# Kernel tuning notes

Measured on AMD Instinct MI355X. Metric: run time of the kernel, lower is better.

The kernel has to match this reference:

```python
import jax, jax.numpy as jnp
from jax import lax
import numpy as np

B, COND_C = 16, 256
IN_C, OUT_C, K = 64, 64, 3
H = W = 128
N_PARAM = K * K * IN_C * OUT_C + OUT_C  # 36928


def setup_inputs() -> dict:
    key = jax.random.key(0)
    k1, k2, k3, k4 = jax.random.split(key, 4)
    x = jax.random.normal(k1, (B, IN_C, H, W), dtype=jnp.float32)
    conditioning = jax.random.normal(k2, (B, COND_C), dtype=jnp.float32)
    # nn.Linear(cond_c, n_param): weight [n_param, cond_c], bias [n_param]
    W_cond = jax.random.normal(k3, (N_PARAM, COND_C), dtype=jnp.float32) * 0.02
    b_cond = jax.random.normal(k4, (N_PARAM,), dtype=jnp.float32) * 0.02
    return {"x": x, "conditioning": conditioning, "W_cond": W_cond, "b_cond": b_cond}


def reference(x, conditioning, W_cond, b_cond):
    # Hypernetwork: Linear + tanh*5 (ConditionerActivation)
    w_b = jnp.tanh(conditioning @ W_cond.T + b_cond) * 5.0  # [B, N_PARAM]
    bias = w_b[:, -OUT_C:]                                   # [B, out_c]
    w = w_b[:, :-OUT_C].reshape(B, OUT_C, IN_C, K, K)        # per-sample OIHW

    def conv_one(xi, wi, bi):
        # xi: [in_c, H, W], wi: [out_c, in_c, K, K], bi: [out_c]
        y = lax.conv_general_dilated(
            xi[None], wi,
            window_strides=(1, 1),
            padding=[(1, 1), (1, 1)],
            dimension_numbers=("NCHW", "OIHW", "NCHW"),
        )[0]
        return y + bi[:, None, None]

    return jax.vmap(conv_one)(x, w, bias)  # [B, out_c, H, W]
```

## Files before the change

kernel.cpp:

```cpp
#include <hip/hip_runtime.h>
#include <math.h>
#include <stdint.h>

#define B_    16
#define CONDC 256
#define ICn   64
#define OCn   64
#define Hn    128
#define Wn    128
#define NW    36864
#define NPARAM 36928

typedef _Float16 half8 __attribute__((ext_vector_type(8)));
typedef _Float16 half4 __attribute__((ext_vector_type(4)));
typedef float f32x4 __attribute__((ext_vector_type(4)));
typedef float f32x16 __attribute__((ext_vector_type(16)));

__device__ inline unsigned pk2(float a, float b) {
    union { _Float16 h[2]; unsigned u; } q;
    q.h[0] = (_Float16)a; q.h[1] = (_Float16)b;
    return q.u;
}

__global__ void transpose_k(const float* __restrict__ x, _Float16* __restrict__ xt) {
    __shared__ unsigned ls[4160];
    const int tid = threadIdx.x;
    const int bx  = blockIdx.x;

    if (bx < 2048) {
        const int b = bx >> 7, y = bx & 127;
        const float* xrow = x + (size_t)b * 1048576 + (size_t)y * 128;

        float4 va[4], vb[4];
        #pragma unroll
        for (int t = 0; t < 4; ++t) {
            int u = t * 256 + tid;
            int icp = u >> 5, xg = u & 31;
            const float* r0 = xrow + (size_t)(2 * icp) * 16384;
            va[t] = *((const float4*)r0 + xg);
            vb[t] = *((const float4*)(r0 + 16384) + xg);
        }
        __builtin_amdgcn_sched_barrier(0);

        #pragma unroll
        for (int t = 0; t < 4; ++t) {
            int u = t * 256 + tid;
            int icp = u >> 5, xg = u & 31;
            unsigned* dst = ls + icp * 130 + 4 * xg;
            *(uint2*)(dst)     = make_uint2(pk2(va[t].x, vb[t].x), pk2(va[t].y, vb[t].y));
            *(uint2*)(dst + 2) = make_uint2(pk2(va[t].z, vb[t].z), pk2(va[t].w, vb[t].w));
        }
        __syncthreads();

        _Float16* rowhalf = xt + (size_t)(b * 130 + y + 1) * 8320;
        #pragma unroll
        for (int t = 0; t < 5; ++t) {
            int u = t * 256 + tid;
            if (u < 1040) {
                int xp = u >> 3, g = u & 7;
                uint4 val = make_uint4(0u, 0u, 0u, 0u);
                if (xp > 0 && xp < 129) {
                    int xx = xp - 1;
                    val.x = ls[(4 * g + 0) * 130 + xx];
                    val.y = ls[(4 * g + 1) * 130 + xx];
                    val.z = ls[(4 * g + 2) * 130 + xx];
                    val.w = ls[(4 * g + 3) * 130 + xx];
                }
                *(uint4*)(rowhalf + (size_t)u * 8) = val;
            }
        }
    } else {
        const int q = bx - 2048;
        const int b = q >> 1, yp = (q & 1) ? 129 : 0;
        _Float16* rowhalf = xt + (size_t)(b * 130 + yp) * 8320;
        uint4 z = make_uint4(0u, 0u, 0u, 0u);
        for (int u = tid; u < 1040; u += 256)
            *(uint4*)(rowhalf + (size_t)u * 8) = z;
    }
}

__global__ __launch_bounds__(256, 4) void gemm_k(const float* __restrict__ cond,
                                                 const float* __restrict__ Wc,
                                                 const float* __restrict__ bc,
                                                 _Float16* __restrict__ wt,
                                                 float* __restrict__ bias) {
    __shared__ _Float16 wl[64 * 280];
    const int tid = threadIdx.x;
    const int pbase = blockIdx.x * 64;

    float4 v[16];
    #pragma unroll
    for (int t = 0; t < 16; ++t) {
        int u = t * 256 + tid;
        int pl = u >> 6, kg = u & 63;
        v[t] = *((const float4*)(Wc + (size_t)(pbase + pl) * 256) + kg);
    }
    __builtin_amdgcn_sched_barrier(0);

    #pragma unroll
    for (int t = 0; t < 16; ++t) {
        int u = t * 256 + tid;
        int pl = u >> 6, kg = u & 63;
        half4 h = { (_Float16)v[t].x, (_Float16)v[t].y, (_Float16)v[t].z, (_Float16)v[t].w };
        *(half4*)(wl + pl * 280 + kg * 4) = h;
    }
    __syncthreads();

    const int w = tid >> 6, l = tid & 63, n = l & 15, r4 = l >> 4;
    const _Float16* arow = wl + (w * 16 + n) * 280 + r4 * 8;
    const float*    crow = cond + n * 256 + r4 * 8;
    f32x4 acc = (f32x4){0.f, 0.f, 0.f, 0.f};
    #pragma unroll
    for (int kk = 0; kk < 8; ++kk) {
        half8 av = *(const half8*)(arow + kk * 32);
        float4 u0 = *(const float4*)(crow + kk * 32);
        float4 u1 = *(const float4*)(crow + kk * 32 + 4);
        half8 bv;
        bv[0] = (_Float16)u0.x; bv[1] = (_Float16)u0.y; bv[2] = (_Float16)u0.z; bv[3] = (_Float16)u0.w;
        bv[4] = (_Float16)u1.x; bv[5] = (_Float16)u1.y; bv[6] = (_Float16)u1.z; bv[7] = (_Float16)u1.w;
        acc = __builtin_amdgcn_mfma_f32_16x16x32_f16(av, bv, acc, 0, 0, 0);
    }
    #pragma unroll
    for (int j = 0; j < 4; ++j) {
        int p = pbase + w * 16 + r4 * 4 + j;
        float vv = tanhf(acc[j] + bc[p]) * 5.0f;
        if (p < NW) {
            int oc = p / 576, rem = p - oc * 576;
            int ic = rem / 9,  t  = rem - ic * 9;
            int icq = ic >> 4, icl = ic & 15;
            wt[((((size_t)n * 4 + icq) * 9 + t) * 64 + oc) * 16 + icl] = (_Float16)vv;
        } else {
            bias[n * 64 + (p - NW)] = vv;
        }
    }
}

__global__ __launch_bounds__(512, 2) void conv_v4(const _Float16* __restrict__ xt,
                                                  const _Float16* __restrict__ wt,
                                                  const float* __restrict__ bias,
                                                  float* __restrict__ out) {
    __shared__ _Float16 xs[2][12288];
    const int tid = threadIdx.x;
    const int l   = tid & 63;
    const int w   = tid >> 6;
    const int px  = l & 31;
    const int jj  = l >> 5;
    const int ot  = w & 1;
    const int rg  = w >> 1;
    const int b   = blockIdx.z;
    const int X0  = blockIdx.x * 32;
    const int Y0g = blockIdx.y * 16;

    const _Float16* xbase = xt + ((size_t)(b * 130 + Y0g) * 130 + X0) * 64;
    const _Float16* wbat  = wt + (size_t)b * 36864 + (size_t)(ot * 32 + px) * 16 + jj * 8;

    int offkw[3];
    #pragma unroll
    for (int kw = 0; kw < 3; ++kw) {
        int c = (px + kw) * 2 + jj;
        offkw[kw] = (c ^ ((c >> 3) & 7)) * 16;
    }
    const int Lb = rg * 4;

    #define STAGEQ(ICQ, BUF) do {                                                       \
        _Pragma("unroll")                                                               \
        for (int it = 0; it < 3; ++it) {                                                \
            int d  = it * 512 + tid;                                                    \
            int dc = d < 1296 ? d : 1295;                                               \
            int row = (int)((unsigned)dc / 72u);                                        \
            int c   = dc - row * 72;                                                    \
            int cs  = c ^ ((c >> 3) & 7);                                               \
            const _Float16* src = xbase + (size_t)row * 8320 + (cs >> 1) * 64           \
                                + (ICQ) * 16 + (cs & 1) * 8;                            \
            __builtin_amdgcn_global_load_lds(                                           \
                (const __attribute__((address_space(1))) void*)src,                     \
                (__attribute__((address_space(3))) void*)((__attribute__((address_space(3))) char*)xs + (BUF) * 24576 + (it * 512 + (tid & ~63)) * 16), \
                16, 0, 0);                                                              \
        } } while (0)

    STAGEQ(0, 0);
    half8 A[2][9];
    #pragma unroll
    for (int t = 0; t < 9; ++t) A[0][t] = *(const half8*)(wbat + t * 1024);

    f32x16 acc[4];
    #pragma unroll
    for (int r = 0; r < 4; ++r) acc[r] = (f32x16){};

    #pragma unroll
    for (int icq = 0; icq < 4; ++icq) {
        const int cur = icq & 1;
        if (icq < 3) {
            STAGEQ(icq + 1, cur ^ 1);
            asm volatile("s_waitcnt vmcnt(3)" ::: "memory");
        } else {
            asm volatile("s_waitcnt vmcnt(0)" ::: "memory");
        }
        __builtin_amdgcn_sched_barrier(0);
        __builtin_amdgcn_s_barrier();
        __builtin_amdgcn_sched_barrier(0);

        if (icq < 3) {
            #pragma unroll
            for (int t = 0; t < 9; ++t)
                A[cur ^ 1][t] = *(const half8*)(wbat + ((icq + 1) * 9 + t) * 1024);
        }

        const char* bufb = (const char*)xs + cur * 24576;
        #pragma unroll
        for (int kw = 0; kw < 3; ++kw) {
            half8 Bf[6];
            #pragma unroll
            for (int iy = 0; iy < 6; ++iy)
                Bf[iy] = *(const half8*)(bufb + (Lb + iy) * 1152 + offkw[kw]);
            #pragma unroll
            for (int iy = 0; iy < 6; ++iy) {
                #pragma unroll
                for (int kh = 0; kh < 3; ++kh) {
                    const int r = iy - kh;
                    if (r >= 0 && r < 4)
                        acc[r] = __builtin_amdgcn_mfma_f32_32x32x16_f16(A[cur][kh * 3 + kw], Bf[iy], acc[r], 0, 0, 0);
                }
            }
        }
        asm volatile("s_waitcnt lgkmcnt(0)" ::: "memory");
        __builtin_amdgcn_sched_barrier(0);
        __builtin_amdgcn_s_barrier();
        __builtin_amdgcn_sched_barrier(0);
    }
    #undef STAGEQ

    const float* bb = bias + b * 64;
    #pragma unroll
    for (int r = 0; r < 4; ++r) {
        const int yo = Y0g + Lb + r;
        float* ob = out + (((size_t)(b * 64 + ot * 32)) * 128 + yo) * 128 + X0 + px;
        #pragma unroll
        for (int reg = 0; reg < 16; ++reg) {
            const int ocl = (reg & 3) + 8 * (reg >> 2) + 4 * jj;
            ob[(size_t)ocl * 16384] = acc[r][reg] + bb[ot * 32 + ocl];
        }
    }
}

__global__ __launch_bounds__(256) void cond_gemm(const float* __restrict__ cond,
                                                 const float* __restrict__ Wc,
                                                 const float* __restrict__ bc,
                                                 float* __restrict__ wb) {
    __shared__ float condl[B_][CONDC + 1];
    __shared__ float Wl[16][CONDC + 1];
    const int tid = threadIdx.x;
    const int p0 = blockIdx.x * 16;
    for (int i = tid; i < B_ * CONDC; i += 256) condl[i >> 8][i & 255] = cond[i];
    for (int i = tid; i < 16 * CONDC; i += 256) {
        int pl = i >> 8, k = i & 255;
        Wl[pl][k] = Wc[(p0 + pl) * CONDC + k];
    }
    __syncthreads();
    const int pl = tid >> 4;
    const int b  = tid & 15;
    float acc = bc[p0 + pl];
    #pragma unroll 8
    for (int k = 0; k < CONDC; ++k) acc += Wl[pl][k] * condl[b][k];
    wb[b * NPARAM + p0 + pl] = tanhf(acc) * 5.0f;
}

#define TS  32
#define OG  8
#define ICC 8
__global__ __launch_bounds__(256) void conv_kernel(const float* __restrict__ x,
                                                   const float* __restrict__ wb,
                                                   float* __restrict__ out) {
    __shared__ float fxs[ICC][TS + 2][TS + 2];
    __shared__ float ws[OG][ICC][9];
    const int tid = threadIdx.x;
    const int b   = blockIdx.z;
    const int ocg = blockIdx.y * OG;
    const int tx0 = (blockIdx.x & 3) * TS;
    const int ty0 = (blockIdx.x >> 2) * TS;
    const int px  = (tid & 15) * 2;
    const int py  = (tid >> 4) * 2;
    float acc[OG][4];
    #pragma unroll
    for (int o = 0; o < OG; ++o)
        #pragma unroll
        for (int q = 0; q < 4; ++q) acc[o][q] = 0.0f;
    const float* wbase = wb + b * NPARAM;
    for (int ic0 = 0; ic0 < ICn; ic0 += ICC) {
        for (int i = tid; i < ICC * (TS + 2) * (TS + 2); i += 256) {
            int icl = i / ((TS + 2) * (TS + 2));
            int rem = i % ((TS + 2) * (TS + 2));
            int yy = rem / (TS + 2), xx = rem % (TS + 2);
            int gy = ty0 - 1 + yy, gx = tx0 - 1 + xx;
            float v = 0.0f;
            if (gy >= 0 && gy < Hn && gx >= 0 && gx < Wn)
                v = x[((b * ICn + ic0 + icl) * Hn + gy) * Wn + gx];
            fxs[icl][yy][xx] = v;
        }
        for (int i = tid; i < OG * ICC * 9; i += 256) {
            int o = i / (ICC * 9), rem = i % (ICC * 9);
            int icl = rem / 9, k = rem % 9;
            ws[o][icl][k] = wbase[((ocg + o) * ICn + ic0 + icl) * 9 + k];
        }
        __syncthreads();
        #pragma unroll
        for (int icl = 0; icl < ICC; ++icl) {
            float xv[4][4];
            #pragma unroll
            for (int dy = 0; dy < 4; ++dy)
                #pragma unroll
                for (int dx = 0; dx < 4; ++dx) xv[dy][dx] = fxs[icl][py + dy][px + dx];
            #pragma unroll
            for (int o = 0; o < OG; ++o)
                #pragma unroll
                for (int kh = 0; kh < 3; ++kh)
                    #pragma unroll
                    for (int kw = 0; kw < 3; ++kw) {
                        float wv = ws[o][icl][kh * 3 + kw];
                        acc[o][0] += xv[kh][kw] * wv;
                        acc[o][1] += xv[kh][kw + 1] * wv;
                        acc[o][2] += xv[kh + 1][kw] * wv;
                        acc[o][3] += xv[kh + 1][kw + 1] * wv;
                    }
        }
        __syncthreads();
    }
    #pragma unroll
    for (int o = 0; o < OG; ++o) {
        float bias = wbase[NW + ocg + o];
        int oc = ocg + o;
        float* obase = out + ((size_t)(b * OCn + oc) * Hn + (ty0 + py)) * Wn + tx0 + px;
        obase[0] = acc[o][0] + bias;
        obase[1] = acc[o][1] + bias;
        obase[Wn] = acc[o][2] + bias;
        obase[Wn + 1] = acc[o][3] + bias;
    }
}

extern "C" void kernel_launch(void* const* d_in, const int* in_sizes, int n_in,
                              void* d_out, int out_size, void* d_ws, size_t ws_size,
                              hipStream_t stream) {
    const float* x    = (const float*)d_in[0];
    const float* cond = (const float*)d_in[1];
    const float* Wc   = (const float*)d_in[2];
    const float* bc   = (const float*)d_in[3];
    float* out = (float*)d_out;

    const size_t WT_BYTES = (size_t)B_ * 9 * 64 * 64 * 2;
    const size_t BIAS_OFF = WT_BYTES;
    const size_t XT_OFF   = 1183744;
    const size_t XT_BYTES = (size_t)B_ * 130 * 130 * 64 * 2 + 32768;
    const size_t NEED     = XT_OFF + XT_BYTES;

    if (ws_size >= NEED) {
        _Float16* wt   = (_Float16*)d_ws;
        float*    bias = (float*)((char*)d_ws + BIAS_OFF);
        _Float16* xt   = (_Float16*)((char*)d_ws + XT_OFF);
        transpose_k<<<dim3(2048 + 32), 256, 0, stream>>>(x, xt);
        gemm_k<<<dim3(577), 256, 0, stream>>>(cond, Wc, bc, wt, bias);
        conv_v4<<<dim3(4, 8, 16), 512, 0, stream>>>(xt, wt, bias, out);
    } else {
        float* wbuf = (float*)d_ws;
        cond_gemm<<<dim3(NPARAM / 16), 256, 0, stream>>>(cond, Wc, bc, wbuf);
        conv_kernel<<<dim3(16, OCn / OG, B_), 256, 0, stream>>>(x, wbuf, out);
    }
}
```

Measured before the change: 69.94 us.

## Shrink conv tiles, triple-buffer input stages, and swizzle block order

The conv kernel now uses 256-thread blocks covering 8 output rows instead of 16, with a three-deep LDS ring of input channel-quarter stages in place of double buffering. All three first stages are prefetched up front, and the four channel quarters are explicitly unrolled with tuned vmcnt waits. A 1D grid with a swizzled block-to-tile mapping spreads consecutive blocks across batches. The goal is better latency hiding and more resident blocks, at the cost of more halo reloads from the smaller tiles and fragile hand-counted waitcnt values.

```diff
diff --git a/kernel.cpp b/kernel.cpp
--- a/kernel.cpp
+++ b/kernel.cpp
@@ -135,11 +135,11 @@
     }
 }
 
-__global__ __launch_bounds__(512, 2) void conv_v4(const _Float16* __restrict__ xt,
+__global__ __launch_bounds__(256, 3) void conv_v5(const _Float16* __restrict__ xt,
                                                   const _Float16* __restrict__ wt,
                                                   const float* __restrict__ bias,
                                                   float* __restrict__ out) {
-    __shared__ _Float16 xs[2][12288];
+    __shared__ _Float16 xs[3 * 6144];
     const int tid = threadIdx.x;
     const int l   = tid & 63;
     const int w   = tid >> 6;
@@ -147,9 +147,11 @@
     const int jj  = l >> 5;
     const int ot  = w & 1;
     const int rg  = w >> 1;
-    const int b   = blockIdx.z;
-    const int X0  = blockIdx.x * 32;
-    const int Y0g = blockIdx.y * 16;
+
+    const int sw = (blockIdx.x & 7) * 128 + (blockIdx.x >> 3);
+    const int Xt = sw & 3, Yt = (sw >> 2) & 15, b = sw >> 6;
+    const int X0  = Xt * 32;
+    const int Y0g = Yt * 8;
 
     const _Float16* xbase = xt + ((size_t)(b * 130 + Y0g) * 130 + X0) * 64;
     const _Float16* wbat  = wt + (size_t)b * 36864 + (size_t)(ot * 32 + px) * 16 + jj * 8;
@@ -165,70 +167,90 @@
     #define STAGEQ(ICQ, BUF) do {                                                       \
         _Pragma("unroll")                                                               \
         for (int it = 0; it < 3; ++it) {                                                \
-            int d  = it * 512 + tid;                                                    \
-            int dc = d < 1296 ? d : 1295;                                               \
-            int row = (int)((unsigned)dc / 72u);                                        \
-            int c   = dc - row * 72;                                                    \
+            int d   = it * 256 + tid;                                                   \
+            int row = (int)((unsigned)d / 72u);                                         \
+            int c   = d - row * 72;                                                     \
             int cs  = c ^ ((c >> 3) & 7);                                               \
             const _Float16* src = xbase + (size_t)row * 8320 + (cs >> 1) * 64           \
                                 + (ICQ) * 16 + (cs & 1) * 8;                            \
             __builtin_amdgcn_global_load_lds(                                           \
                 (const __attribute__((address_space(1))) void*)src,                     \
-                (__attribute__((address_space(3))) void*)((__attribute__((address_space(3))) char*)xs + (BUF) * 24576 + (it * 512 + (tid & ~63)) * 16), \
+                (__attribute__((address_space(3))) void*)((__attribute__((address_space(3))) char*)xs + (BUF) * 12288 + (it * 256 + (tid & ~63)) * 16), \
                 16, 0, 0);                                                              \
         } } while (0)
 
-    STAGEQ(0, 0);
+    #define LOADA(AIDX, ICQ) do {                                                       \
+        _Pragma("unroll")                                                               \
+        for (int t = 0; t < 9; ++t)                                                     \
+            A[AIDX][t] = *(const half8*)(wbat + (size_t)((ICQ) * 9 + t) * 1024);        \
+        } while (0)
+
+    #define COMPUTE(AIDX, BUF) do {                                                     \
+        const char* bufb = (const char*)xs + (BUF) * 12288;                             \
+        _Pragma("unroll")                                                               \
+        for (int kw = 0; kw < 3; ++kw) {                                                \
+            half8 Bf[6];                                                                \
+            _Pragma("unroll")                                                           \
+            for (int iy = 0; iy < 6; ++iy)                                              \
+                Bf[iy] = *(const half8*)(bufb + (Lb + iy) * 1152 + offkw[kw]);          \
+            _Pragma("unroll")                                                           \
+            for (int iy = 0; iy < 6; ++iy) {                                            \
+                _Pragma("unroll")                                                       \
+                for (int kh = 0; kh < 3; ++kh) {                                        \
+                    const int r = iy - kh;                                              \
+                    if (r >= 0 && r < 4)                                                \
+                        acc[r] = __builtin_amdgcn_mfma_f32_32x32x16_f16(A[AIDX][kh * 3 + kw], Bf[iy], acc[r], 0, 0, 0); \
+                } } } } while (0)
+
     half8 A[2][9];
-    #pragma unroll
-    for (int t = 0; t < 9; ++t) A[0][t] = *(const half8*)(wbat + t * 1024);
-
     f32x16 acc[4];
     #pragma unroll
     for (int r = 0; r < 4; ++r) acc[r] = (f32x16){};
 
-    #pragma unroll
-    for (int icq = 0; icq < 4; ++icq) {
-        const int cur = icq & 1;
-        if (icq < 3) {
-            STAGEQ(icq + 1, cur ^ 1);
-            asm volatile("s_waitcnt vmcnt(3)" ::: "memory");
-        } else {
-            asm volatile("s_waitcnt vmcnt(0)" ::: "memory");
-        }
-        __builtin_amdgcn_sched_barrier(0);
-        __builtin_amdgcn_s_barrier();
-        __builtin_amdgcn_sched_barrier(0);
-
-        if (icq < 3) {
-            #pragma unroll
-            for (int t = 0; t < 9; ++t)
-                A[cur ^ 1][t] = *(const half8*)(wbat + ((icq + 1) * 9 + t) * 1024);
-        }
-
-        const char* bufb = (const char*)xs + cur * 24576;
-        #pragma unroll
-        for (int kw = 0; kw < 3; ++kw) {
-            half8 Bf[6];
-            #pragma unroll
-            for (int iy = 0; iy < 6; ++iy)
-                Bf[iy] = *(const half8*)(bufb + (Lb + iy) * 1152 + offkw[kw]);
-            #pragma unroll
-            for (int iy = 0; iy < 6; ++iy) {
-                #pragma unroll
-                for (int kh = 0; kh < 3; ++kh) {
-                    const int r = iy - kh;
-                    if (r >= 0 && r < 4)
-                        acc[r] = __builtin_amdgcn_mfma_f32_32x32x16_f16(A[cur][kh * 3 + kw], Bf[iy], acc[r], 0, 0, 0);
-                }
-            }
-        }
-        asm volatile("s_waitcnt lgkmcnt(0)" ::: "memory");
-        __builtin_amdgcn_sched_barrier(0);
-        __builtin_amdgcn_s_barrier();
-        __builtin_amdgcn_sched_barrier(0);
-    }
+    LOADA(0, 0);
+    __builtin_amdgcn_sched_barrier(0);
+    STAGEQ(0, 0); STAGEQ(1, 1); STAGEQ(2, 2);
+    __builtin_amdgcn_sched_barrier(0);
+
+    LOADA(1, 1);
+    __builtin_amdgcn_sched_barrier(0);
+    asm volatile("s_waitcnt vmcnt(15)" ::: "memory");
+    __builtin_amdgcn_sched_barrier(0);
+    __builtin_amdgcn_s_barrier();
+    __builtin_amdgcn_sched_barrier(0);
+    COMPUTE(0, 0);
+    asm volatile("s_waitcnt lgkmcnt(0)" ::: "memory");
+    __builtin_amdgcn_sched_barrier(0);
+    __builtin_amdgcn_s_barrier();
+    __builtin_amdgcn_sched_barrier(0);
+    STAGEQ(3, 0);
+    __builtin_amdgcn_sched_barrier(0);
+
+    LOADA(0, 2);
+    __builtin_amdgcn_sched_barrier(0);
+    asm volatile("s_waitcnt vmcnt(12)" ::: "memory");
+    __builtin_amdgcn_sched_barrier(0);
+    __builtin_amdgcn_s_barrier();
+    __builtin_amdgcn_sched_barrier(0);
+    COMPUTE(1, 1);
+
+    LOADA(1, 3);
+    __builtin_amdgcn_sched_barrier(0);
+    asm volatile("s_waitcnt vmcnt(9)" ::: "memory");
+    __builtin_amdgcn_sched_barrier(0);
+    __builtin_amdgcn_s_barrier();
+    __builtin_amdgcn_sched_barrier(0);
+    COMPUTE(0, 2);
+
+    asm volatile("s_waitcnt vmcnt(0)" ::: "memory");
+    __builtin_amdgcn_sched_barrier(0);
+    __builtin_amdgcn_s_barrier();
+    __builtin_amdgcn_sched_barrier(0);
+    COMPUTE(1, 0);
+
     #undef STAGEQ
+    #undef LOADA
+    #undef COMPUTE
 
     const float* bb = bias + b * 64;
     #pragma unroll
@@ -358,7 +380,7 @@
         _Float16* xt   = (_Float16*)((char*)d_ws + XT_OFF);
         transpose_k<<<dim3(2048 + 32), 256, 0, stream>>>(x, xt);
         gemm_k<<<dim3(577), 256, 0, stream>>>(cond, Wc, bc, wt, bias);
-        conv_v4<<<dim3(4, 8, 16), 512, 0, stream>>>(xt, wt, bias, out);
+        conv_v5<<<dim3(1024), 256, 0, stream>>>(xt, wt, bias, out);
     } else {
         float* wbuf = (float*)d_ws;
         cond_gemm<<<dim3(NPARAM / 16), 256, 0, stream>>>(cond, Wc, bc, wbuf);
```

Result: faster. 62.77 us (-10.2%).
